# Kernel optimization log

Measured on AMD Instinct MI355X. Metric: run time of the kernel, lower is better.

## Reference

```python
import jax, jax.numpy as jnp
import numpy as np

B, L, S, DIM, NH = 4, 1024, 1024, 1024, 16
DH = DIM // NH


def setup_inputs() -> dict:
    key = jax.random.key(0)
    ks = jax.random.split(key, 16)
    std = 0.02
    inp = {
        'q': jax.random.normal(ks[0], (B, L, DIM), jnp.float32),
        'k': jax.random.normal(ks[1], (B, S, DIM), jnp.float32),
        'v': jax.random.normal(ks[2], (B, S, DIM), jnp.float32),
        'attn_mask': jax.random.bernoulli(ks[3], 0.9, (B, L, S)),
        'pos_bias': jax.random.normal(ks[4], (B, NH, L, S), jnp.float32),
        'Wq': jax.random.normal(ks[5], (DIM, DIM), jnp.float32) * std,
        'bq': jnp.zeros((DIM,), jnp.float32),
        'Wk': jax.random.normal(ks[6], (DIM, DIM), jnp.float32) * std,
        'bk': jnp.zeros((DIM,), jnp.float32),
        'Wv': jax.random.normal(ks[7], (DIM, DIM), jnp.float32) * std,
        'bv': jnp.zeros((DIM,), jnp.float32),
        'Wp': jax.random.normal(ks[8], (DIM, DIM), jnp.float32) * std,
        'bp': jnp.zeros((DIM,), jnp.float32),
        'is_causal': 1,
    }
    return inp


def _attention(q, k, v, attn_mask, pos_bias, Wq, bq, Wk, bk, Wv, bv, Wp, bp, is_causal):
    b, l, _ = q.shape
    s = k.shape[1]
    qh = (q @ Wq + bq).reshape(b, l, NH, DH)   # (B,L,nH,dh)
    kh = (k @ Wk + bk).reshape(b, s, NH, DH)
    vh = (v @ Wv + bv).reshape(b, s, NH, DH)

    mask = attn_mask  # (B,L,S) bool
    if is_causal:
        causal = jnp.tril(jnp.ones((l, l), dtype=bool))
        causal = jnp.pad(causal, ((0, 0), (s - l, 0)), constant_values=True)  # (L,S)
        mask = mask & causal[None]
    # rows with no allowed key attend everywhere (matches torch row-fix)
    row_any = mask.any(axis=-1, keepdims=True)
    mask = jnp.where(row_any, mask, True)

    bias = jnp.where(mask[:, None, :, :], pos_bias, -jnp.inf)  # (B,nH,L,S)
    scale = 1.0 / np.sqrt(DH).astype(np.float32)
    scores = jnp.einsum('blhd,bshd->bhls', qh, kh) * scale + bias
    attn = jax.nn.softmax(scores, axis=-1)
    o = jnp.einsum('bhls,bshd->blhd', attn, vh).reshape(b, l, NH * DH)
    return o @ Wp + bp


def reference(q, k, v, attn_mask, pos_bias, Wq, bq, Wk, bk, Wv, bv, Wp, bp, is_causal):
    return _attention(q, k, v, attn_mask, pos_bias, Wq, bq, Wk, bk, Wv, bv, Wp, bp, is_causal)
```

## Files before the change

### kernel.cpp

```cpp
#include <hip/hip_runtime.h>
#include <hip/hip_bf16.h>

typedef __hip_bfloat16 bf16;
typedef __attribute__((ext_vector_type(4))) float  floatx4;
typedef __attribute__((ext_vector_type(8))) short  short8;
typedef __attribute__((ext_vector_type(8))) __bf16 bf16x8;

constexpr int Bc = 4, Lc = 1024, Sc = 1024, DIMc = 1024, NHc = 16, DHc = 64;

template <typename V>
__device__ auto mfma_bf16_sel(V a, V b, floatx4 c, int)
    -> decltype(__builtin_amdgcn_mfma_f32_16x16x32_bf16(a, b, c, 0, 0, 0)) {
  return __builtin_amdgcn_mfma_f32_16x16x32_bf16(a, b, c, 0, 0, 0);
}
template <typename V>
__device__ floatx4 mfma_bf16_sel(V a, V b, floatx4 c, long) {
  bf16x8 a2 = __builtin_bit_cast(bf16x8, a);
  bf16x8 b2 = __builtin_bit_cast(bf16x8, b);
  return __builtin_amdgcn_mfma_f32_16x16x32_bf16(a2, b2, c, 0, 0, 0);
}
__device__ inline floatx4 mfma_bf16(short8 a, short8 b, floatx4 c) {
  return mfma_bf16_sel(a, b, c, 0);
}

union U8 { uint4 u; bf16 h[8]; };

__device__ inline U8 load8(const float* p) {
    float4 f0 = ((const float4*)p)[0];
    float4 f1 = ((const float4*)p)[1];
    U8 t;
    t.h[0] = __float2bfloat16(f0.x); t.h[1] = __float2bfloat16(f0.y);
    t.h[2] = __float2bfloat16(f0.z); t.h[3] = __float2bfloat16(f0.w);
    t.h[4] = __float2bfloat16(f1.x); t.h[5] = __float2bfloat16(f1.y);
    t.h[6] = __float2bfloat16(f1.z); t.h[7] = __float2bfloat16(f1.w);
    return t;
}
__device__ inline U8 load8(const bf16* p) {
    U8 t; t.u = *(const uint4*)p; return t;
}
__device__ inline void store_elem(float* p, float v) { *p = v; }
__device__ inline void store_elem(bf16*  p, float v) { *p = __float2bfloat16(v); }

template <typename TA, typename TO>
__global__ __launch_bounds__(256)
void gemm_bias_kernel(const TA* __restrict__ A, const float* __restrict__ W,
                      const float* __restrict__ bias, TO* __restrict__ out,
                      int M, int N, int K, int mode)
{
    __shared__ bf16 As[64][32];
    __shared__ bf16 Bt[64][32];

    const int tid  = threadIdx.x;
    const int wave = tid >> 6;
    const int lane = tid & 63;
    const int m0 = blockIdx.x * 64;
    const int n0 = blockIdx.y * 64;

    floatx4 acc[4];
    #pragma unroll
    for (int t = 0; t < 4; ++t) acc[t] = (floatx4){0.f, 0.f, 0.f, 0.f};

    const int ar = tid >> 2;
    const int ac = (tid & 3) << 3;
    const int wk = tid >> 3;
    const int wn = (tid & 7) << 3;

    const int mrow = (wave << 4) + (lane & 15);
    const int kk   = (lane >> 4) << 3;

    for (int k0 = 0; k0 < K; k0 += 32) {
        U8 at = load8(A + (size_t)(m0 + ar) * K + k0 + ac);
        *(uint4*)(&As[ar][ac]) = at.u;
        U8 wt = load8(W + (size_t)(k0 + wk) * N + n0 + wn);
        #pragma unroll
        for (int j = 0; j < 8; ++j) Bt[wn + j][wk] = wt.h[j];
        __syncthreads();

        short8 a8 = *(const short8*)(&As[mrow][kk]);
        #pragma unroll
        for (int t = 0; t < 4; ++t) {
            short8 b8 = *(const short8*)(&Bt[(t << 4) + (lane & 15)][kk]);
            acc[t] = mfma_bf16(a8, b8, acc[t]);
        }
        __syncthreads();
    }

    #pragma unroll
    for (int t = 0; t < 4; ++t) {
        const int col = n0 + (t << 4) + (lane & 15);
        const float bval = bias[col];
        #pragma unroll
        for (int r = 0; r < 4; ++r) {
            const int row = m0 + (wave << 4) + ((lane >> 4) << 2) + r;
            const float v = acc[t][r] + bval;
            const int bb = row >> 10, ll = row & (Lc - 1);
            const int hh = col >> 6,  dd = col & 63;
            size_t idx;
            if (mode == 0)      idx = (size_t)row * N + col;
            else if (mode == 1) idx = (((size_t)(bb * NHc + hh) * Lc + ll) * DHc) + dd;
            else                idx = (((size_t)(bb * NHc + hh) * DHc + dd) * Sc) + ll;
            store_elem(out + idx, v);
        }
    }
}

constexpr int PADk = 72;

__global__ __launch_bounds__(256)
void flash_attn_kernel(const bf16* __restrict__ qh, const bf16* __restrict__ kh,
                       const bf16* __restrict__ vt, const int* __restrict__ mask,
                       const float* __restrict__ pos_bias,
                       const int* __restrict__ is_causal_p, bf16* __restrict__ o)
{
    __shared__ bf16 Ks[64 * PADk];
    __shared__ bf16 Vs[64 * PADk];
    __shared__ bf16 Pw[4][16 * PADk];
    __shared__ int rowany[64];
    __shared__ int hasfix_s;

    const int tid  = threadIdx.x;
    const int lane = tid & 63;
    const int wave = tid >> 6;
    const int n = lane & 15;
    const int g = lane >> 4;

    const int qt = blockIdx.x & 15;
    const int bh = blockIdx.x >> 4;
    const int h  = bh & (NHc - 1);
    const int b  = bh >> 4;
    const int l0 = qt * 64;
    const bool causal = (is_causal_p[0] != 0);

    if (tid < 64) rowany[tid] = 0;
    if (tid == 0) hasfix_s = 0;
    __syncthreads();
    {
        const int row = tid >> 2, part = tid & 3;
        const int l = l0 + row;
        const int limit = causal ? l : (Sc - 1);
        const int* mrow = mask + ((size_t)b * Lc + l) * Sc;
        int any = 0;
        for (int s = part * 256; s < part * 256 + 256; ++s) {
            if (s <= limit && mrow[s] != 0) { any = 1; break; }
        }
        if (any) atomicOr(&rowany[row], 1);
    }
    __syncthreads();
    if (tid < 64 && rowany[tid] == 0) atomicOr(&hasfix_s, 1);
    __syncthreads();
    const bool hasfix = (hasfix_s != 0);

    const int qrow_frag = l0 + wave * 16 + n;
    const bf16* qp = qh + ((size_t)bh * Lc + qrow_frag) * DHc;
    const short8 qf0 = *(const short8*)(qp + g * 8);
    const short8 qf1 = *(const short8*)(qp + 32 + g * 8);

    floatx4 oacc[4];
    #pragma unroll
    for (int t = 0; t < 4; ++t) oacc[t] = (floatx4){0.f, 0.f, 0.f, 0.f};
    float m_run[4], l_run[4];
    #pragma unroll
    for (int r = 0; r < 4; ++r) { m_run[r] = -3.0e38f; l_run[r] = 0.f; }

    int nchunk = Sc / 64;
    if (causal && !hasfix) nchunk = qt + 1;

    for (int c = 0; c < nchunk; ++c) {
        const int s0 = c * 64;
        __syncthreads();
        #pragma unroll
        for (int it = 0; it < 2; ++it) {
            const int e  = tid * 8 + it * 2048;
            const int r0 = e >> 6, c0 = e & 63;
            *(uint4*)(Ks + r0 * PADk + c0) =
                *(const uint4*)(kh + ((size_t)bh * Sc + s0 + r0) * DHc + c0);
            *(uint4*)(Vs + r0 * PADk + c0) =
                *(const uint4*)(vt + ((size_t)bh * DHc + r0) * Sc + s0 + c0);
        }
        __syncthreads();

        float bi[4][4]; int mk[4][4];
        #pragma unroll
        for (int r = 0; r < 4; ++r) {
            const int l = l0 + wave * 16 + g * 4 + r;
            const size_t mb = ((size_t)b  * Lc + l) * Sc + s0 + n;
            const size_t pb = ((size_t)bh * Lc + l) * Sc + s0 + n;
            #pragma unroll
            for (int t = 0; t < 4; ++t) {
                mk[r][t] = mask[mb + 16 * t];
                bi[r][t] = pos_bias[pb + 16 * t];
            }
        }

        floatx4 scv[4];
        #pragma unroll
        for (int t = 0; t < 4; ++t) scv[t] = (floatx4){0.f, 0.f, 0.f, 0.f};
        #pragma unroll
        for (int t = 0; t < 4; ++t) {
            short8 kb0 = *(const short8*)(Ks + (16 * t + n) * PADk + g * 8);
            short8 kb1 = *(const short8*)(Ks + (16 * t + n) * PADk + 32 + g * 8);
            scv[t] = mfma_bf16(qf0, kb0, scv[t]);
            scv[t] = mfma_bf16(qf1, kb1, scv[t]);
        }

        #pragma unroll
        for (int r = 0; r < 4; ++r) {
            const int row = wave * 16 + g * 4 + r;
            const int l = l0 + row;
            const int limit = causal ? l : (Sc - 1);
            const bool fix = (rowany[row] == 0);
            float vals[4];
            #pragma unroll
            for (int t = 0; t < 4; ++t) {
                const int s = s0 + 16 * t + n;
                const bool ok = fix || (s <= limit && mk[r][t] != 0);
                vals[t] = ok ? scv[t][r] * 0.125f + bi[r][t] : -3.0e38f;
            }
            float cm = fmaxf(fmaxf(vals[0], vals[1]), fmaxf(vals[2], vals[3]));
            cm = fmaxf(cm, __shfl_xor(cm, 1));
            cm = fmaxf(cm, __shfl_xor(cm, 2));
            cm = fmaxf(cm, __shfl_xor(cm, 4));
            cm = fmaxf(cm, __shfl_xor(cm, 8));
            const float mnew = fmaxf(m_run[r], cm);
            const float alpha = __expf(m_run[r] - mnew);
            float csum = 0.f;
            #pragma unroll
            for (int t = 0; t < 4; ++t) {
                const float p = (vals[t] < -1.0e37f) ? 0.f : __expf(vals[t] - mnew);
                csum += p;
                Pw[wave][row % 16 * PADk + 16 * t + n] = __float2bfloat16(p);
            }
            csum += __shfl_xor(csum, 1);
            csum += __shfl_xor(csum, 2);
            csum += __shfl_xor(csum, 4);
            csum += __shfl_xor(csum, 8);
            l_run[r] = l_run[r] * alpha + csum;
            m_run[r] = mnew;
            #pragma unroll
            for (int t = 0; t < 4; ++t) oacc[t][r] *= alpha;
        }
        __syncthreads();

        #pragma unroll
        for (int sc2 = 0; sc2 < 2; ++sc2) {
            short8 pa = *(const short8*)(Pw[wave] + n * PADk + sc2 * 32 + g * 8);
            #pragma unroll
            for (int t = 0; t < 4; ++t) {
                short8 vb = *(const short8*)(Vs + (16 * t + n) * PADk + sc2 * 32 + g * 8);
                oacc[t] = mfma_bf16(pa, vb, oacc[t]);
            }
        }
    }

    #pragma unroll
    for (int r = 0; r < 4; ++r) {
        const int l = l0 + wave * 16 + g * 4 + r;
        const float inv = 1.f / l_run[r];
        #pragma unroll
        for (int t = 0; t < 4; ++t) {
            const int d = 16 * t + n;
            o[((size_t)(b * Lc + l)) * DIMc + h * DHc + d] =
                __float2bfloat16(oacc[t][r] * inv);
        }
    }
}

extern "C" void kernel_launch(void* const* d_in, const int* in_sizes, int n_in,
                              void* d_out, int out_size, void* d_ws, size_t ws_size,
                              hipStream_t stream)
{
    (void)in_sizes; (void)n_in; (void)out_size; (void)ws_size;

    const float* q        = (const float*)d_in[0];
    const float* k        = (const float*)d_in[1];
    const float* v        = (const float*)d_in[2];
    const int*   mask     = (const int*)d_in[3];
    const float* pos_bias = (const float*)d_in[4];
    const float* Wq = (const float*)d_in[5];
    const float* bq = (const float*)d_in[6];
    const float* Wk = (const float*)d_in[7];
    const float* bk = (const float*)d_in[8];
    const float* Wv = (const float*)d_in[9];
    const float* bv = (const float*)d_in[10];
    const float* Wp = (const float*)d_in[11];
    const float* bp = (const float*)d_in[12];
    const int*   is_causal = (const int*)d_in[13];

    const size_t per = (size_t)Bc * NHc * Lc * DHc;
    bf16* qh = (bf16*)d_ws;
    bf16* kh = qh + per;
    bf16* vt = kh + per;
    bf16* oh = vt + per;
    float* outp = (float*)d_out;

    const int Mrows = Bc * Lc;
    dim3 gg(Mrows / 64, DIMc / 64);
    dim3 bb(256);

    gemm_bias_kernel<float, bf16><<<gg, bb, 0, stream>>>(q, Wq, bq, qh, Mrows, DIMc, DIMc, 1);
    gemm_bias_kernel<float, bf16><<<gg, bb, 0, stream>>>(k, Wk, bk, kh, Mrows, DIMc, DIMc, 1);
    gemm_bias_kernel<float, bf16><<<gg, bb, 0, stream>>>(v, Wv, bv, vt, Mrows, DIMc, DIMc, 2);

    flash_attn_kernel<<<(Bc * NHc) * (Lc / 64), bb, 0, stream>>>(
        qh, kh, vt, mask, pos_bias, is_causal, oh);

    gemm_bias_kernel<bf16, float><<<gg, bb, 0, stream>>>(oh, Wp, bp, outp, Mrows, DIMc, DIMc, 0);
}
```

Baseline: 677.3 us.

## Pre-convert inputs and transpose weights to bf16, use 128x128 GEMM tiles

Adds a prep kernel that casts q/k/v to bf16 and writes bf16 transposed copies of all four weight matrices. The projection GEMMs are replaced by a kernel with 128x128 output tiles and a K step of 64, where each wave computes a 64x64 sub-tile from 16 MFMA accumulators. The aim is to raise data reuse per shared-memory load and drop the per-iteration fp32 conversion and scattered transpose stores in the GEMM inner loop. In exchange there is an extra launch plus workspace traffic, and the per-call weight transpose costs time each call.

Measured after the change: 600.5 us. 1.13x faster.

```diff
diff --git a/kernel.cpp b/kernel.cpp
--- a/kernel.cpp
+++ b/kernel.cpp
@@ -35,71 +35,131 @@
     t.h[6] = __float2bfloat16(f1.z); t.h[7] = __float2bfloat16(f1.w);
     return t;
 }
-__device__ inline U8 load8(const bf16* p) {
-    U8 t; t.u = *(const uint4*)p; return t;
-}
 __device__ inline void store_elem(float* p, float v) { *p = v; }
 __device__ inline void store_elem(bf16*  p, float v) { *p = __float2bfloat16(v); }
 
-template <typename TA, typename TO>
 __global__ __launch_bounds__(256)
-void gemm_bias_kernel(const TA* __restrict__ A, const float* __restrict__ W,
-                      const float* __restrict__ bias, TO* __restrict__ out,
-                      int M, int N, int K, int mode)
+void prep_kernel(const float* __restrict__ q, const float* __restrict__ k,
+                 const float* __restrict__ v,
+                 const float* __restrict__ Wq, const float* __restrict__ Wk,
+                 const float* __restrict__ Wv, const float* __restrict__ Wp,
+                 bf16* __restrict__ qb, bf16* __restrict__ kb,
+                 bf16* __restrict__ vb,
+                 bf16* __restrict__ wqt, bf16* __restrict__ wkt,
+                 bf16* __restrict__ wvt, bf16* __restrict__ wpt)
 {
-    __shared__ bf16 As[64][32];
-    __shared__ bf16 Bt[64][32];
+    __shared__ float tile[64][68];
+    const int tid = threadIdx.x;
+    int blk = blockIdx.x;
+
+    if (blk < 6144) {
+        const float* src = (blk < 2048) ? q : (blk < 4096) ? k : v;
+        bf16*        dst = (blk < 2048) ? qb : (blk < 4096) ? kb : vb;
+        const int off = (blk & 2047) * 2048 + tid * 8;
+        U8 t = load8(src + off);
+        *(uint4*)(dst + off) = t.u;
+    } else {
+        blk -= 6144;
+        const int w  = blk >> 8, t2 = blk & 255;
+        const float* W  = (w == 0) ? Wq : (w == 1) ? Wk : (w == 2) ? Wv : Wp;
+        bf16*        Wt = (w == 0) ? wqt : (w == 1) ? wkt : (w == 2) ? wvt : wpt;
+        const int tk = (t2 >> 4) << 6;
+        const int tn = (t2 & 15) << 6;
+        #pragma unroll
+        for (int i = 0; i < 4; ++i) {
+            const int r = (tid >> 4) + i * 16;
+            const int c = (tid & 15) << 2;
+            *(float4*)(&tile[r][c]) =
+                *(const float4*)(W + (size_t)(tk + r) * DIMc + tn + c);
+        }
+        __syncthreads();
+        #pragma unroll
+        for (int j = 0; j < 2; ++j) {
+            const int nn = tid >> 2;
+            const int kc = (tid & 3) + j * 4;
+            U8 o;
+            #pragma unroll
+            for (int u = 0; u < 8; ++u)
+                o.h[u] = __float2bfloat16(tile[kc * 8 + u][nn]);
+            *(uint4*)(Wt + (size_t)(tn + nn) * DIMc + tk + kc * 8) = o.u;
+        }
+    }
+}
+
+constexpr int GPAD = 72;
+
+template <typename TO>
+__global__ __launch_bounds__(256)
+void gemm_bt_kernel(const bf16* __restrict__ A, const bf16* __restrict__ Bt,
+                    const float* __restrict__ bias, TO* __restrict__ out,
+                    int mode)
+{
+    __shared__ bf16 As[128 * GPAD];
+    __shared__ bf16 Bs[128 * GPAD];
 
     const int tid  = threadIdx.x;
     const int wave = tid >> 6;
     const int lane = tid & 63;
-    const int m0 = blockIdx.x * 64;
-    const int n0 = blockIdx.y * 64;
-
-    floatx4 acc[4];
-    #pragma unroll
-    for (int t = 0; t < 4; ++t) acc[t] = (floatx4){0.f, 0.f, 0.f, 0.f};
-
-    const int ar = tid >> 2;
-    const int ac = (tid & 3) << 3;
-    const int wk = tid >> 3;
-    const int wn = (tid & 7) << 3;
-
-    const int mrow = (wave << 4) + (lane & 15);
-    const int kk   = (lane >> 4) << 3;
-
-    for (int k0 = 0; k0 < K; k0 += 32) {
-        U8 at = load8(A + (size_t)(m0 + ar) * K + k0 + ac);
-        *(uint4*)(&As[ar][ac]) = at.u;
-        U8 wt = load8(W + (size_t)(k0 + wk) * N + n0 + wn);
-        #pragma unroll
-        for (int j = 0; j < 8; ++j) Bt[wn + j][wk] = wt.h[j];
-        __syncthreads();
-
-        short8 a8 = *(const short8*)(&As[mrow][kk]);
-        #pragma unroll
-        for (int t = 0; t < 4; ++t) {
-            short8 b8 = *(const short8*)(&Bt[(t << 4) + (lane & 15)][kk]);
-            acc[t] = mfma_bf16(a8, b8, acc[t]);
-        }
-        __syncthreads();
-    }
-
-    #pragma unroll
-    for (int t = 0; t < 4; ++t) {
-        const int col = n0 + (t << 4) + (lane & 15);
+    const int n = lane & 15, g = lane >> 4;
+    const int m0 = blockIdx.x * 128;
+    const int n0 = blockIdx.y * 128;
+    const int wq_m = (wave & 1) * 64, wq_n = (wave >> 1) * 64;
+
+    floatx4 acc[4][4];
+    #pragma unroll
+    for (int a = 0; a < 4; ++a)
+        #pragma unroll
+        for (int b2 = 0; b2 < 4; ++b2)
+            acc[a][b2] = (floatx4){0.f, 0.f, 0.f, 0.f};
+
+    const int srow   = tid >> 3;
+    const int schunk = (tid & 7) * 8;
+
+    for (int k0 = 0; k0 < DIMc; k0 += 64) {
+        #pragma unroll
+        for (int i = 0; i < 4; ++i) {
+            const int r = srow + i * 32;
+            *(uint4*)(&As[r * GPAD + schunk]) =
+                *(const uint4*)(A + (size_t)(m0 + r) * DIMc + k0 + schunk);
+            *(uint4*)(&Bs[r * GPAD + schunk]) =
+                *(const uint4*)(Bt + (size_t)(n0 + r) * DIMc + k0 + schunk);
+        }
+        __syncthreads();
+        #pragma unroll
+        for (int ks = 0; ks < 2; ++ks) {
+            short8 af[4], bf_[4];
+            #pragma unroll
+            for (int t = 0; t < 4; ++t) {
+                af[t]  = *(const short8*)(&As[(wq_m + t * 16 + n) * GPAD + ks * 32 + g * 8]);
+                bf_[t] = *(const short8*)(&Bs[(wq_n + t * 16 + n) * GPAD + ks * 32 + g * 8]);
+            }
+            #pragma unroll
+            for (int tm = 0; tm < 4; ++tm)
+                #pragma unroll
+                for (int tn = 0; tn < 4; ++tn)
+                    acc[tm][tn] = mfma_bf16(af[tm], bf_[tn], acc[tm][tn]);
+        }
+        __syncthreads();
+    }
+
+    #pragma unroll
+    for (int tn = 0; tn < 4; ++tn) {
+        const int col = n0 + wq_n + tn * 16 + n;
         const float bval = bias[col];
         #pragma unroll
-        for (int r = 0; r < 4; ++r) {
-            const int row = m0 + (wave << 4) + ((lane >> 4) << 2) + r;
-            const float v = acc[t][r] + bval;
-            const int bb = row >> 10, ll = row & (Lc - 1);
-            const int hh = col >> 6,  dd = col & 63;
-            size_t idx;
-            if (mode == 0)      idx = (size_t)row * N + col;
-            else if (mode == 1) idx = (((size_t)(bb * NHc + hh) * Lc + ll) * DHc) + dd;
-            else                idx = (((size_t)(bb * NHc + hh) * DHc + dd) * Sc) + ll;
-            store_elem(out + idx, v);
+        for (int tm = 0; tm < 4; ++tm) {
+            #pragma unroll
+            for (int r = 0; r < 4; ++r) {
+                const int row = m0 + wq_m + tm * 16 + g * 4 + r;
+                const float vv = acc[tm][tn][r] + bval;
+                const int bb = row >> 10, ll = row & (Lc - 1);
+                const int hh = col >> 6,  dd = col & 63;
+                size_t idx;
+                if (mode == 0)      idx = (size_t)row * DIMc + col;
+                else if (mode == 1) idx = (((size_t)(bb * NHc + hh) * Lc + ll) * DHc) + dd;
+                else                idx = (((size_t)(bb * NHc + hh) * DHc + dd) * Sc) + ll;
+                store_elem(out + idx, vv);
+            }
         }
     }
 }
@@ -287,22 +347,32 @@
     const int*   is_causal = (const int*)d_in[13];
 
     const size_t per = (size_t)Bc * NHc * Lc * DHc;
-    bf16* qh = (bf16*)d_ws;
-    bf16* kh = qh + per;
-    bf16* vt = kh + per;
-    bf16* oh = vt + per;
+    const size_t wsz = (size_t)DIMc * DIMc;
+    bf16* qh  = (bf16*)d_ws;
+    bf16* kh  = qh + per;
+    bf16* vt  = kh + per;
+    bf16* oh  = vt + per;
+    bf16* qb  = oh + per;
+    bf16* kb  = qb + per;
+    bf16* vb  = kb + per;
+    bf16* wqt = vb + per;
+    bf16* wkt = wqt + wsz;
+    bf16* wvt = wkt + wsz;
+    bf16* wpt = wvt + wsz;
     float* outp = (float*)d_out;
 
-    const int Mrows = Bc * Lc;
-    dim3 gg(Mrows / 64, DIMc / 64);
     dim3 bb(256);
 
-    gemm_bias_kernel<float, bf16><<<gg, bb, 0, stream>>>(q, Wq, bq, qh, Mrows, DIMc, DIMc, 1);
-    gemm_bias_kernel<float, bf16><<<gg, bb, 0, stream>>>(k, Wk, bk, kh, Mrows, DIMc, DIMc, 1);
-    gemm_bias_kernel<float, bf16><<<gg, bb, 0, stream>>>(v, Wv, bv, vt, Mrows, DIMc, DIMc, 2);
+    prep_kernel<<<7168, bb, 0, stream>>>(q, k, v, Wq, Wk, Wv, Wp,
+                                         qb, kb, vb, wqt, wkt, wvt, wpt);
+
+    dim3 gg(32, 8);
+    gemm_bt_kernel<bf16><<<gg, bb, 0, stream>>>(qb, wqt, bq, qh, 1);
+    gemm_bt_kernel<bf16><<<gg, bb, 0, stream>>>(kb, wkt, bk, kh, 1);
+    gemm_bt_kernel<bf16><<<gg, bb, 0, stream>>>(vb, wvt, bv, vt, 2);
 
     flash_attn_kernel<<<(Bc * NHc) * (Lc / 64), bb, 0, stream>>>(
         qh, kh, vt, mask, pos_bias, is_causal, oh);
 
-    gemm_bias_kernel<bf16, float><<<gg, bb, 0, stream>>>(oh, Wp, bp, outp, Mrows, DIMc, DIMc, 0);
-}
+    gemm_bt_kernel<float><<<gg, bb, 0, stream>>>(oh, wpt, bp, outp, 0);
+}
```
